# Kernel optimization log

Measured on AMD Instinct MI355X. Metric: run time of the kernel, lower is better.

Reference implementation:

```python
import math
import jax, jax.numpy as jnp
import numpy as np

B, T, E, H = 1, 2048, 2048, 16
D = E // H // 2  # head_dim = 64
DEPTH = 12
LAMBDA_INIT = 0.8 - 0.6 * math.exp(-0.3 * DEPTH)
EPS = 1e-5
NEG = -1e30


def rotary_cos_sin(seqlen, dim):
    # matches flash-attn RotaryEmbedding: inv_freq over even indices, base 10000
    inv_freq = 1.0 / (10000.0 ** (jnp.arange(0, dim, 2, dtype=jnp.float32) / dim))
    t = jnp.arange(seqlen, dtype=jnp.float32)
    freqs = jnp.outer(t, inv_freq)  # [T, D/2]
    return jnp.cos(freqs), jnp.sin(freqs)


def apply_rotary_interleaved(x, cos, sin):
    # x: [B, T, nH, D]; rotate interleaved pairs (x0,x1),(x2,x3),...
    x1 = x[..., 0::2]
    x2 = x[..., 1::2]
    c = cos[None, :, None, :]
    s = sin[None, :, None, :]
    o1 = x1 * c - x2 * s
    o2 = x1 * s + x2 * c
    return jnp.stack([o1, o2], axis=-1).reshape(x.shape)


def causal_attn_pair(q, k, v1, v2, mask, scale):
    # q,k,v*: [B, T, H, D]; shared softmax over (q,k), applied to both v1 and v2
    s = jnp.einsum('bthd,bshd->bhts', q, k) * scale
    s = jnp.where(mask, s, NEG)
    a = jax.nn.softmax(s, axis=-1)
    o1 = jnp.einsum('bhts,bshd->bthd', a, v1)
    o2 = jnp.einsum('bhts,bshd->bthd', a, v2)
    return jnp.concatenate([o1, o2], axis=-1)  # [B, T, H, 2D]


def setup_inputs() -> dict:
    key = jax.random.key(0)
    ks = jax.random.split(key, 10)
    return {
        'query': jax.random.normal(ks[0], (B, T, E), dtype=jnp.float32),
        'Wq': jax.random.normal(ks[1], (E, E), dtype=jnp.float32) * 0.02,
        'Wk': jax.random.normal(ks[2], (E, E), dtype=jnp.float32) * 0.02,
        'Wv': jax.random.normal(ks[3], (E, E), dtype=jnp.float32) * 0.02,
        'Wout': jax.random.normal(ks[4], (E, E), dtype=jnp.float32) * 0.02,
        'lambda_q1': jax.random.normal(ks[5], (D,), dtype=jnp.float32) * 0.1,
        'lambda_k1': jax.random.normal(ks[6], (D,), dtype=jnp.float32) * 0.1,
        'lambda_q2': jax.random.normal(ks[7], (D,), dtype=jnp.float32) * 0.1,
        'lambda_k2': jax.random.normal(ks[8], (D,), dtype=jnp.float32) * 0.1,
        'rms_weight': jnp.ones((2 * D,), dtype=jnp.float32),
    }


def reference(query, Wq, Wk, Wv, Wout, lambda_q1, lambda_k1, lambda_q2, lambda_k2, rms_weight):
    bsz, tgt_len, embed_dim = query.shape
    cos, sin = rotary_cos_sin(tgt_len, D)
    scale = D ** (-0.5)
    mask = jnp.tril(jnp.ones((tgt_len, tgt_len), dtype=bool))[None, None]

    q = (query @ Wq).reshape(bsz, tgt_len, 2 * H, D)
    k = (query @ Wk).reshape(bsz, tgt_len, 2 * H, D)
    v = (query @ Wv).reshape(bsz, tgt_len, H, 2, D)

    q = apply_rotary_emb = apply_rotary_interleaved(q, cos, sin)
    k = apply_rotary_interleaved(k, cos, sin)

    q = q.reshape(bsz, tgt_len, H, 2, D)
    k = k.reshape(bsz, tgt_len, H, 2, D)
    q1, q2 = q[:, :, :, 0], q[:, :, :, 1]
    k1, k2 = k[:, :, :, 0], k[:, :, :, 1]
    v1, v2 = v[:, :, :, 0], v[:, :, :, 1]

    attn1 = causal_attn_pair(q1, k1, v1, v2, mask, scale)  # [B,T,H,2D]
    attn2 = causal_attn_pair(q2, k2, v1, v2, mask, scale)

    lambda_1 = jnp.exp(jnp.sum(lambda_q1 * lambda_k1))
    lambda_2 = jnp.exp(jnp.sum(lambda_q2 * lambda_k2))
    lambda_full = lambda_1 - lambda_2 + LAMBDA_INIT

    f1 = jnp.fft.rfft(attn1, axis=1)
    f2 = jnp.fft.rfft(attn2, axis=1)
    attn_freq = f1 - lambda_full * f2

    n_freq = attn_freq.shape[1]
    sigma = 0.3 / 2.0  # cutoff_ratio / 2, gaussian window
    x = jnp.linspace(0.0, 1.0, n_freq)
    filt = jnp.exp(-0.5 * (x / sigma) ** 2)
    attn_freq = attn_freq * filt[None, :, None, None]

    attn = jnp.fft.irfft(attn_freq, n=tgt_len, axis=1)  # [B,T,H,2D]

    # RMSNorm over last dim (2*head_dim) with affine weight
    attn = attn * jax.lax.rsqrt(jnp.mean(attn * attn, axis=-1, keepdims=True) + EPS) * rms_weight
    attn = attn * (1.0 - LAMBDA_INIT)

    attn = attn.reshape(bsz, tgt_len, H * 2 * D)
    return attn @ Wout
```

## Files before the change

### kernel.cpp

```cpp
#include <hip/hip_runtime.h>
#include <math.h>

#define LAMBDA_INIT_F 0.7836057665316245f
#define ONE_MINUS_LI  0.2163942334683755f

typedef unsigned short ushort_t;
typedef unsigned int   uint32;
typedef unsigned long long u64;
typedef __attribute__((ext_vector_type(8))) short short8;
typedef __attribute__((ext_vector_type(4))) float f32x4;

__device__ __forceinline__ ushort_t f2bf(float f) {
    union { float f; uint32 u; } x; x.f = f;
    uint32 r = (x.u + 0x7fffu + ((x.u >> 16) & 1u)) >> 16;
    return (ushort_t)r;
}

__device__ __forceinline__ void gld16(ushort_t* lds, const ushort_t* g) {
    __builtin_amdgcn_global_load_lds(
        (const __attribute__((address_space(1))) uint32*)g,
        (__attribute__((address_space(3))) uint32*)lds,
        16, 0, 0);
}

__global__ __launch_bounds__(64) void lambda_kernel(
    const float* __restrict__ lq1, const float* __restrict__ lk1,
    const float* __restrict__ lq2, const float* __restrict__ lk2,
    float* __restrict__ lam)
{
    int l = threadIdx.x;
    float p1 = lq1[l] * lk1[l];
    float p2 = lq2[l] * lk2[l];
    for (int off = 32; off; off >>= 1) {
        p1 += __shfl_down(p1, off);
        p2 += __shfl_down(p2, off);
    }
    if (l == 0) lam[0] = expf(p1) - expf(p2) + LAMBDA_INIT_F;
}

__global__ __launch_bounds__(256) void gfilt_kernel(float* __restrict__ g)
{
    __shared__ float red[4];
    const int j = blockIdx.x;
    int tau = j - 64;
    int ta = tau < 0 ? -tau : tau;
    const int tid = threadIdx.x;
    float acc = 0.0f;
    for (int k = tid; k <= 1024; k += 256) {
        float w = (k == 0 || k == 1024) ? 1.0f : 2.0f;
        float r = (float)k * (1.0f / 153.6f);
        float f = expf(-0.5f * r * r);
        int m = (k * ta) & 2047;
        float ang = (float)m * 3.0679615757712823e-3f;
        acc += w * f * cosf(ang);
    }
    for (int off = 32; off; off >>= 1) acc += __shfl_down(acc, off);
    if ((tid & 63) == 0) red[tid >> 6] = acc;
    __syncthreads();
    if (tid == 0)
        g[j] = (red[0] + red[1] + red[2] + red[3]) * (1.0f / 2048.0f);
}

__global__ __launch_bounds__(256) void rottab(float* __restrict__ ct, float* __restrict__ st)
{
    int id = blockIdx.x * 256 + threadIdx.x;
    int t = id >> 5, i = id & 31;
    double inv = exp(-0.28782313662425575 * (double)i);
    double a = (double)t * inv;
    ct[id] = (float)cos(a);
    st[id] = (float)sin(a);
}

__global__ __launch_bounds__(256) void cvt_bf16(const float* __restrict__ s, ushort_t* __restrict__ d)
{
    int i = (blockIdx.x * 256 + threadIdx.x) * 8;
    float4 a = *(const float4*)(s + i);
    float4 b = *(const float4*)(s + i + 4);
    uint4 pk;
    pk.x = (uint32)f2bf(a.x) | ((uint32)f2bf(a.y) << 16);
    pk.y = (uint32)f2bf(a.z) | ((uint32)f2bf(a.w) << 16);
    pk.z = (uint32)f2bf(b.x) | ((uint32)f2bf(b.y) << 16);
    pk.w = (uint32)f2bf(b.z) | ((uint32)f2bf(b.w) << 16);
    *(uint4*)(d + i) = pk;
}

__global__ __launch_bounds__(256) void wtrans(
    const float* __restrict__ Wq, const float* __restrict__ Wk,
    const float* __restrict__ Wv, const float* __restrict__ Wo,
    ushort_t* __restrict__ Tq, ushort_t* __restrict__ Tk,
    ushort_t* __restrict__ Tv, ushort_t* __restrict__ To)
{
    int z = blockIdx.z;
    const float* S = (z == 0) ? Wq : (z == 1) ? Wk : (z == 2) ? Wv : Wo;
    ushort_t* Dt = (z == 0) ? Tq : (z == 1) ? Tk : (z == 2) ? Tv : To;
    bool perm = (z < 2);
    __shared__ float Ls[64 * 65];
    const int tid = threadIdx.x;
    const int n0 = blockIdx.x * 64, k0 = blockIdx.y * 64;
    #pragma unroll
    for (int it = 0; it < 4; ++it) {
        int kk = it * 16 + (tid >> 4);
        int nn = (tid & 15) * 4;
        float4 v = *(const float4*)(S + (size_t)(k0 + kk) * 2048 + n0 + nn);
        Ls[(nn + 0) * 65 + kk] = v.x;
        Ls[(nn + 1) * 65 + kk] = v.y;
        Ls[(nn + 2) * 65 + kk] = v.z;
        Ls[(nn + 3) * 65 + kk] = v.w;
    }
    __syncthreads();
    int nl = tid >> 2, kc = (tid & 3) * 16;
    int ng = n0 + nl;
    int nd = perm ? ((ng & ~63) | ((ng & 1) << 5) | ((ng & 63) >> 1)) : ng;
    uint4 p0, p1;
    const float* row = Ls + nl * 65 + kc;
    p0.x = (uint32)f2bf(row[0])  | ((uint32)f2bf(row[1])  << 16);
    p0.y = (uint32)f2bf(row[2])  | ((uint32)f2bf(row[3])  << 16);
    p0.z = (uint32)f2bf(row[4])  | ((uint32)f2bf(row[5])  << 16);
    p0.w = (uint32)f2bf(row[6])  | ((uint32)f2bf(row[7])  << 16);
    p1.x = (uint32)f2bf(row[8])  | ((uint32)f2bf(row[9])  << 16);
    p1.y = (uint32)f2bf(row[10]) | ((uint32)f2bf(row[11]) << 16);
    p1.z = (uint32)f2bf(row[12]) | ((uint32)f2bf(row[13]) << 16);
    p1.w = (uint32)f2bf(row[14]) | ((uint32)f2bf(row[15]) << 16);
    *(uint4*)(Dt + (size_t)nd * 2048 + k0 + kc) = p0;
    *(uint4*)(Dt + (size_t)nd * 2048 + k0 + kc + 8) = p1;
}

__global__ __launch_bounds__(256) void gemm_qkv(
    const ushort_t* __restrict__ A, const ushort_t* __restrict__ WT,
    ushort_t* __restrict__ q1, ushort_t* __restrict__ q2,
    ushort_t* __restrict__ k1, ushort_t* __restrict__ k2,
    ushort_t* __restrict__ v1T, ushort_t* __restrict__ v2T,
    const float* __restrict__ ctab, const float* __restrict__ stab)
{
    __shared__ ushort_t As[8192];
    __shared__ ushort_t Bs[8192];
    const int tid = threadIdx.x;
    const int w = tid >> 6, lane = tid & 63;
    const int quad = lane >> 4, l15 = lane & 15;
    const int wr = w >> 1, wc = w & 1;
    const int rb = blockIdx.y * 128, cb = blockIdx.x * 128;

    f32x4 acc[4][4];
    #pragma unroll
    for (int i = 0; i < 4; ++i)
        #pragma unroll
        for (int j = 0; j < 4; ++j) acc[i][j] = (f32x4)0.0f;

    for (int k0 = 0; k0 < 2048; k0 += 64) {
        #pragma unroll
        for (int u = 0; u < 4; ++u) {
            int off = (w * 4 + u) * 512;
            int Lc = (off >> 3) + lane;
            int row = Lc >> 3, cc = (Lc & 7) ^ (row & 7);
            gld16(As + off, A + (size_t)(rb + row) * 2048 + k0 + cc * 8);
            gld16(Bs + off, WT + (size_t)(cb + row) * 2048 + k0 + cc * 8);
        }
        __syncthreads();
        #pragma unroll
        for (int ks = 0; ks < 2; ++ks) {
            short8 af[4], bfr[4];
            #pragma unroll
            for (int mi = 0; mi < 4; ++mi) {
                int r = wr * 64 + mi * 16 + l15;
                af[mi] = *(const short8*)(As + r * 64 + ((ks * 4 + quad) ^ (r & 7)) * 8);
            }
            #pragma unroll
            for (int nj = 0; nj < 4; ++nj) {
                int r = wc * 64 + nj * 16 + l15;
                bfr[nj] = *(const short8*)(Bs + r * 64 + ((ks * 4 + quad) ^ (r & 7)) * 8);
            }
            #pragma unroll
            for (int mi = 0; mi < 4; ++mi)
                #pragma unroll
                for (int nj = 0; nj < 4; ++nj)
                    acc[mi][nj] = __builtin_amdgcn_mfma_f32_16x16x32_bf16(
                        af[mi], bfr[nj], acc[mi][nj], 0, 0, 0);
        }
        __syncthreads();
    }

    const int region = cb >> 11;
    const int nloc = cb & 2047;
    if (region < 2) {
        int head2 = (nloc + wc * 64) >> 6;
        ushort_t* b1 = region ? k1 : q1;
        ushort_t* b2 = region ? k2 : q2;
        ushort_t* dst = ((head2 & 1) ? b2 : b1) + (size_t)(head2 >> 1) * 2048 * 64;
        #pragma unroll
        for (int mi = 0; mi < 4; ++mi)
            #pragma unroll
            for (int r = 0; r < 4; ++r) {
                int t = rb + wr * 64 + mi * 16 + quad * 4 + r;
                const float* ctr = ctab + t * 32;
                const float* str = stab + t * 32;
                #pragma unroll
                for (int nj = 0; nj < 2; ++nj) {
                    int i = nj * 16 + l15;
                    float c = ctr[i], s = str[i];
                    float x1 = acc[mi][nj][r], x2 = acc[mi][nj + 2][r];
                    dst[(size_t)t * 64 + i]      = f2bf(x1 * c - x2 * s);
                    dst[(size_t)t * 64 + 32 + i] = f2bf(x1 * s + x2 * c);
                }
            }
    } else {
        #pragma unroll
        for (int mi = 0; mi < 4; ++mi)
            #pragma unroll
            for (int nj = 0; nj < 4; ++nj) {
                int cg = nloc + wc * 64 + nj * 16 + l15;
                int hh = cg >> 7, pr = (cg >> 6) & 1, d = cg & 63;
                int tb = rb + wr * 64 + mi * 16 + quad * 4;
                ushort_t* dst = (pr ? v2T : v1T) + ((size_t)(hh * 64 + d)) * 2048 + tb;
                u64 pk = (u64)f2bf(acc[mi][nj][0])
                       | ((u64)f2bf(acc[mi][nj][1]) << 16)
                       | ((u64)f2bf(acc[mi][nj][2]) << 32)
                       | ((u64)f2bf(acc[mi][nj][3]) << 48);
                *(u64*)dst = pk;
            }
    }
}

#define PSTRIDE 88

__device__ __forceinline__ void attn_step(
    const ushort_t* __restrict__ Kb, const ushort_t* __restrict__ V1b,
    const ushort_t* __restrict__ V2b, ushort_t* __restrict__ pw,
    const short8* qb, f32x4* O, float& m_i, float& l_i,
    int quad, int l15, int row_l, bool diag)
{
    f32x4 s[4];
    #pragma unroll
    for (int j = 0; j < 4; ++j) s[j] = (f32x4)0.0f;
    #pragma unroll
    for (int ks = 0; ks < 2; ++ks)
        #pragma unroll
        for (int j = 0; j < 4; ++j) {
            int r = j * 16 + l15;
            short8 kf = *(const short8*)(Kb + r * 64 + ((ks * 4 + quad) ^ (r & 7)) * 8);
            s[j] = __builtin_amdgcn_mfma_f32_16x16x32_bf16(kf, qb[ks], s[j], 0, 0, 0);
        }
    float pv[16];
    float mx = -1e30f;
    #pragma unroll
    for (int j = 0; j < 4; ++j)
        #pragma unroll
        for (int r = 0; r < 4; ++r) {
            float v = s[j][r] * 0.125f;
            if (diag) {
                int kp = j * 16 + quad * 4 + r;
                v = (kp <= row_l) ? v : -1e30f;
            }
            pv[j * 4 + r] = v;
            mx = fmaxf(mx, v);
        }
    mx = fmaxf(mx, __shfl_xor(mx, 16));
    mx = fmaxf(mx, __shfl_xor(mx, 32));
    float newm = fmaxf(m_i, mx);
    float alpha = __expf(m_i - newm);
    float sum = 0.0f;
    ushort_t pb[16];
    #pragma unroll
    for (int i = 0; i < 16; ++i) {
        float p = __expf(pv[i] - newm);
        sum += p;
        pb[i] = f2bf(p);
    }
    sum += __shfl_xor(sum, 16);
    sum += __shfl_xor(sum, 32);
    l_i = l_i * alpha + sum;
    m_i = newm;
    #pragma unroll
    for (int j = 0; j < 4; ++j) {
        u64 pk = (u64)pb[j * 4] | ((u64)pb[j * 4 + 1] << 16)
               | ((u64)pb[j * 4 + 2] << 32) | ((u64)pb[j * 4 + 3] << 48);
        *(u64*)(pw + l15 * PSTRIDE + j * 16 + quad * 4) = pk;
    }
    float av0 = __shfl(alpha, quad * 4 + 0);
    float av1 = __shfl(alpha, quad * 4 + 1);
    float av2 = __shfl(alpha, quad * 4 + 2);
    float av3 = __shfl(alpha, quad * 4 + 3);
    #pragma unroll
    for (int nt = 0; nt < 8; ++nt) {
        O[nt][0] *= av0; O[nt][1] *= av1; O[nt][2] *= av2; O[nt][3] *= av3;
    }
    #pragma unroll
    for (int ks = 0; ks < 2; ++ks) {
        short8 pf = *(const short8*)(pw + l15 * PSTRIDE + ks * 32 + quad * 8);
        #pragma unroll
        for (int nt = 0; nt < 8; ++nt) {
            const ushort_t* Vs = (nt < 4) ? V1b : V2b;
            int d = (nt & 3) * 16 + l15;
            short8 vf = *(const short8*)(Vs + d * 64 + ((ks * 4 + quad) ^ (d & 7)) * 8);
            O[nt] = __builtin_amdgcn_mfma_f32_16x16x32_bf16(pf, vf, O[nt], 0, 0, 0);
        }
    }
}

__global__ __launch_bounds__(256) void attn_pipe(
    const ushort_t* __restrict__ q1, const ushort_t* __restrict__ k1,
    const ushort_t* __restrict__ q2, const ushort_t* __restrict__ k2,
    const ushort_t* __restrict__ v1T, const ushort_t* __restrict__ v2T,
    float* __restrict__ X, const float* __restrict__ lam_ptr)
{
    __shared__ ushort_t Tt[4][4096];
    __shared__ ushort_t Ps[4][2][16 * PSTRIDE];

    const int tid = threadIdx.x;
    const int w = tid >> 6, lane = tid & 63;
    const int quad = lane >> 4, l15 = lane & 15;
    const int b = blockIdx.x;
    const int h = b & 15;
    const int qt = 31 - (b >> 4);
    const float lam = lam_ptr[0];
    const int row_l = w * 16 + l15;

    const ushort_t* k1h = k1 + (size_t)h * 2048 * 64;
    const ushort_t* k2h = k2 + (size_t)h * 2048 * 64;
    const ushort_t* v1h = v1T + (size_t)h * 64 * 2048;
    const ushort_t* v2h = v2T + (size_t)h * 64 * 2048;

    short8 qb1[2], qb2[2];
    {
        const ushort_t* q1p = q1 + ((size_t)h * 2048 + qt * 64 + w * 16 + l15) * 64 + quad * 8;
        const ushort_t* q2p = q2 + ((size_t)h * 2048 + qt * 64 + w * 16 + l15) * 64 + quad * 8;
        qb1[0] = *(const short8*)(q1p);      qb1[1] = *(const short8*)(q1p + 32);
        qb2[0] = *(const short8*)(q2p);      qb2[1] = *(const short8*)(q2p + 32);
    }

    int ci[2], koff[2], voff[2];
    #pragma unroll
    for (int u = 0; u < 2; ++u) {
        ci[u] = tid * 2 + u;
        int row = ci[u] >> 3, cc = (ci[u] & 7) ^ (row & 7);
        koff[u] = row * 64 + cc * 8;
        voff[u] = row * 2048 + cc * 8;
    }

    short8 sK1[2], sK2[2], sV1[2], sV2[2];

    #pragma unroll
    for (int u = 0; u < 2; ++u) {
        sK1[u] = *(const short8*)(k1h + koff[u]);
        sK2[u] = *(const short8*)(k2h + koff[u]);
        sV1[u] = *(const short8*)(v1h + voff[u]);
        sV2[u] = *(const short8*)(v2h + voff[u]);
    }
    #pragma unroll
    for (int u = 0; u < 2; ++u) {
        *(short8*)(&Tt[0][ci[u] * 8]) = sK1[u];
        *(short8*)(&Tt[1][ci[u] * 8]) = sK2[u];
        *(short8*)(&Tt[2][ci[u] * 8]) = sV1[u];
        *(short8*)(&Tt[3][ci[u] * 8]) = sV2[u];
    }
    __syncthreads();

    f32x4 O1[8], O2[8];
    #pragma unroll
    for (int i = 0; i < 8; ++i) { O1[i] = (f32x4)0.0f; O2[i] = (f32x4)0.0f; }
    float m1 = -1e30f, l1 = 0.0f, m2 = -1e30f, l2 = 0.0f;

    for (int kt = 0; kt <= qt; ++kt) {
        if (kt < qt) {
            int kb = (kt + 1) * 4096, vb = (kt + 1) * 64;
            #pragma unroll
            for (int u = 0; u < 2; ++u) {
                sK1[u] = *(const short8*)(k1h + kb + koff[u]);
                sK2[u] = *(const short8*)(k2h + kb + koff[u]);
                sV1[u] = *(const short8*)(v1h + vb + voff[u]);
                sV2[u] = *(const short8*)(v2h + vb + voff[u]);
            }
        }
        const bool diag = (kt == qt);
        attn_step(Tt[0], Tt[2], Tt[3], &Ps[w][0][0], qb1, O1, m1, l1, quad, l15, row_l, diag);
        attn_step(Tt[1], Tt[2], Tt[3], &Ps[w][1][0], qb2, O2, m2, l2, quad, l15, row_l, diag);
        __syncthreads();
        if (kt < qt) {
            #pragma unroll
            for (int u = 0; u < 2; ++u) {
                *(short8*)(&Tt[0][ci[u] * 8]) = sK1[u];
                *(short8*)(&Tt[1][ci[u] * 8]) = sK2[u];
                *(short8*)(&Tt[2][ci[u] * 8]) = sV1[u];
                *(short8*)(&Tt[3][ci[u] * 8]) = sV2[u];
            }
            __syncthreads();
        }
    }

    float r10 = 1.0f / __shfl(l1, quad * 4 + 0);
    float r11 = 1.0f / __shfl(l1, quad * 4 + 1);
    float r12 = 1.0f / __shfl(l1, quad * 4 + 2);
    float r13 = 1.0f / __shfl(l1, quad * 4 + 3);
    float r20 = lam / __shfl(l2, quad * 4 + 0);
    float r21 = lam / __shfl(l2, quad * 4 + 1);
    float r22 = lam / __shfl(l2, quad * 4 + 2);
    float r23 = lam / __shfl(l2, quad * 4 + 3);
    int tb = qt * 64 + w * 16 + quad * 4;
    #pragma unroll
    for (int nt = 0; nt < 8; ++nt) {
        int col = h * 128 + nt * 16 + l15;
        X[(size_t)(tb + 0) * 2048 + col] = O1[nt][0] * r10 - O2[nt][0] * r20;
        X[(size_t)(tb + 1) * 2048 + col] = O1[nt][1] * r11 - O2[nt][1] * r21;
        X[(size_t)(tb + 2) * 2048 + col] = O1[nt][2] * r12 - O2[nt][2] * r22;
        X[(size_t)(tb + 3) * 2048 + col] = O1[nt][3] * r13 - O2[nt][3] * r23;
    }
}

__global__ __launch_bounds__(256) void conv_t(
    const float* __restrict__ X, const float* __restrict__ g, float* __restrict__ Y)
{
    __shared__ float Xs[192 * 64];
    __shared__ float gs[129];
    const int tid = threadIdx.x;
    const int c0 = blockIdx.x * 64, t0 = blockIdx.y * 64;
    const int c = tid & 63, tg = tid >> 6;
    for (int j = tg; j < 192; j += 4)
        Xs[j * 64 + c] = X[(size_t)((t0 - 64 + j) & 2047) * 2048 + c0 + c];
    if (tid < 129) gs[tid] = g[tid];
    __syncthreads();
    float accv[16];
    #pragma unroll
    for (int i = 0; i < 16; ++i) accv[i] = 0.0f;
    const int tl0 = tg * 16;
    for (int tap = 0; tap < 129; ++tap) {
        float gv = gs[tap];
        int base = (tl0 + 128 - tap) * 64 + c;
        #pragma unroll
        for (int i = 0; i < 16; ++i) accv[i] += gv * Xs[base + i * 64];
    }
    #pragma unroll
    for (int i = 0; i < 16; ++i)
        Y[(size_t)(t0 + tl0 + i) * 2048 + c0 + c] = accv[i];
}

__global__ __launch_bounds__(64) void rms_bf(
    const float* __restrict__ Y, const float* __restrict__ wgt, ushort_t* __restrict__ yb)
{
    int grp = blockIdx.x;
    int t = grp >> 4, hh = grp & 15, l = threadIdx.x;
    size_t base = (size_t)t * 2048 + hh * 128;
    float a = Y[base + l];
    float b = Y[base + 64 + l];
    float ss = a * a + b * b;
    for (int off = 32; off; off >>= 1) ss += __shfl_down(ss, off);
    ss = __shfl(ss, 0);
    float r = rsqrtf(ss * (1.0f / 128.0f) + 1e-5f) * ONE_MINUS_LI;
    yb[base + l]      = f2bf(a * r * wgt[l]);
    yb[base + 64 + l] = f2bf(b * r * wgt[64 + l]);
}

__global__ __launch_bounds__(256) void gemm_out(
    const ushort_t* __restrict__ A, const ushort_t* __restrict__ BT,
    float* __restrict__ C)
{
    __shared__ ushort_t As[4096];
    __shared__ ushort_t Bs[8192];
    const int tid = threadIdx.x;
    const int w = tid >> 6, lane = tid & 63;
    const int quad = lane >> 4, l15 = lane & 15;
    const int wr = w >> 1, wc = w & 1;
    const int rb = blockIdx.y * 64, cb = blockIdx.x * 128;

    f32x4 acc[2][4];
    #pragma unroll
    for (int i = 0; i < 2; ++i)
        #pragma unroll
        for (int j = 0; j < 4; ++j) acc[i][j] = (f32x4)0.0f;

    for (int k0 = 0; k0 < 2048; k0 += 64) {
        #pragma unroll
        for (int u = 0; u < 2; ++u) {
            int off = (w * 2 + u) * 512;
            int Lc = (off >> 3) + lane;
            int row = Lc >> 3, cc = (Lc & 7) ^ (row & 7);
            gld16(As + off, A + (size_t)(rb + row) * 2048 + k0 + cc * 8);
        }
        #pragma unroll
        for (int u = 0; u < 4; ++u) {
            int off = (w * 4 + u) * 512;
            int Lc = (off >> 3) + lane;
            int row = Lc >> 3, cc = (Lc & 7) ^ (row & 7);
            gld16(Bs + off, BT + (size_t)(cb + row) * 2048 + k0 + cc * 8);
        }
        __syncthreads();
        #pragma unroll
        for (int ks = 0; ks < 2; ++ks) {
            short8 af[2], bfr[4];
            #pragma unroll
            for (int mi = 0; mi < 2; ++mi) {
                int r = wr * 32 + mi * 16 + l15;
                af[mi] = *(const short8*)(As + r * 64 + ((ks * 4 + quad) ^ (r & 7)) * 8);
            }
            #pragma unroll
            for (int nj = 0; nj < 4; ++nj) {
                int r = wc * 64 + nj * 16 + l15;
                bfr[nj] = *(const short8*)(Bs + r * 64 + ((ks * 4 + quad) ^ (r & 7)) * 8);
            }
            #pragma unroll
            for (int mi = 0; mi < 2; ++mi)
                #pragma unroll
                for (int nj = 0; nj < 4; ++nj)
                    acc[mi][nj] = __builtin_amdgcn_mfma_f32_16x16x32_bf16(
                        af[mi], bfr[nj], acc[mi][nj], 0, 0, 0);
        }
        __syncthreads();
    }

    #pragma unroll
    for (int mi = 0; mi < 2; ++mi)
        #pragma unroll
        for (int nj = 0; nj < 4; ++nj) {
            int cg = cb + wc * 64 + nj * 16 + l15;
            #pragma unroll
            for (int r = 0; r < 4; ++r) {
                int t = rb + wr * 32 + mi * 16 + quad * 4 + r;
                C[(size_t)t * 2048 + cg] = acc[mi][nj][r];
            }
        }
}

extern "C" void kernel_launch(void* const* d_in, const int* in_sizes, int n_in,
                              void* d_out, int out_size, void* d_ws, size_t ws_size,
                              hipStream_t stream)
{
    const float* query = (const float*)d_in[0];
    const float* Wq    = (const float*)d_in[1];
    const float* Wk    = (const float*)d_in[2];
    const float* Wv    = (const float*)d_in[3];
    const float* Wout  = (const float*)d_in[4];
    const float* lq1   = (const float*)d_in[5];
    const float* lk1   = (const float*)d_in[6];
    const float* lq2   = (const float*)d_in[7];
    const float* lk2   = (const float*)d_in[8];
    const float* rmsw  = (const float*)d_in[9];
    float* out = (float*)d_out;

    const size_t MB = 1ull << 20;
    char* W = (char*)d_ws;
    ushort_t* WqT   = (ushort_t*)(W + 0 * MB);
    ushort_t* WkT   = (ushort_t*)(W + 8 * MB);
    ushort_t* WvT   = (ushort_t*)(W + 16 * MB);
    ushort_t* WoutT = (ushort_t*)(W + 24 * MB);
    ushort_t* qb    = (ushort_t*)(W + 32 * MB);
    ushort_t* q1    = (ushort_t*)(W + 40 * MB);
    ushort_t* q2    = (ushort_t*)(W + 44 * MB);
    ushort_t* k1    = (ushort_t*)(W + 48 * MB);
    ushort_t* k2    = (ushort_t*)(W + 52 * MB);
    ushort_t* v1T   = (ushort_t*)(W + 56 * MB);
    ushort_t* v2T   = (ushort_t*)(W + 60 * MB);
    float*    X     = (float*)   (W + 64 * MB);
    float*    Y     = (float*)   (W + 32 * MB);
    ushort_t* ybf   = (ushort_t*)(W + 48 * MB);
    float*    ctab  = (float*)   (W + 80 * MB);
    float*    stab  = (float*)   (W + 80 * MB + 256 * 1024);
    float*    gbuf  = (float*)   (W + 80 * MB + 512 * 1024);
    float*    lam   = (float*)   (W + 80 * MB + 520 * 1024);

    lambda_kernel<<<1, 64, 0, stream>>>(lq1, lk1, lq2, lk2, lam);
    gfilt_kernel<<<129, 256, 0, stream>>>(gbuf);
    rottab<<<256, 256, 0, stream>>>(ctab, stab);
    cvt_bf16<<<2048, 256, 0, stream>>>(query, qb);
    wtrans<<<dim3(32, 32, 4), 256, 0, stream>>>(Wq, Wk, Wv, Wout, WqT, WkT, WvT, WoutT);

    gemm_qkv<<<dim3(48, 16), 256, 0, stream>>>(qb, WqT, q1, q2, k1, k2, v1T, v2T, ctab, stab);

    attn_pipe<<<512, 256, 0, stream>>>(q1, k1, q2, k2, v1T, v2T, X, lam);

    conv_t<<<dim3(32, 32), 256, 0, stream>>>(X, gbuf, Y);
    rms_bf<<<32768, 64, 0, stream>>>(Y, rmsw, ybf);

    gemm_out<<<dim3(16, 32), 256, 0, stream>>>(ybf, WoutT, out);
}
```

Baseline: 364.4 us.

## Split dual attention streams across separate wave groups in a 512-thread block

The attention kernel now runs 8 waves per block. Waves 0-3 compute the q1/k1 softmax path and waves 4-7 compute the q2/k2 path, where before each wave ran both paths back to back. The two results are combined through LDS at the end. The query-tile ordering also changes so that the second half of the blocks takes short tiles first, and the softmax packing is fused to avoid extra register arrays. The aim is more parallel waves and lower register pressure per wave, at the cost of an extra LDS round trip and a block barrier at the end.

```diff
diff --git a/kernel.cpp b/kernel.cpp
--- a/kernel.cpp
+++ b/kernel.cpp
@@ -239,7 +239,6 @@
             short8 kf = *(const short8*)(Kb + r * 64 + ((ks * 4 + quad) ^ (r & 7)) * 8);
             s[j] = __builtin_amdgcn_mfma_f32_16x16x32_bf16(kf, qb[ks], s[j], 0, 0, 0);
         }
-    float pv[16];
     float mx = -1e30f;
     #pragma unroll
     for (int j = 0; j < 4; ++j)
@@ -250,7 +249,7 @@
                 int kp = j * 16 + quad * 4 + r;
                 v = (kp <= row_l) ? v : -1e30f;
             }
-            pv[j * 4 + r] = v;
+            s[j][r] = v;
             mx = fmaxf(mx, v);
         }
     mx = fmaxf(mx, __shfl_xor(mx, 16));
@@ -258,23 +257,21 @@
     float newm = fmaxf(m_i, mx);
     float alpha = __expf(m_i - newm);
     float sum = 0.0f;
-    ushort_t pb[16];
-    #pragma unroll
-    for (int i = 0; i < 16; ++i) {
-        float p = __expf(pv[i] - newm);
-        sum += p;
-        pb[i] = f2bf(p);
+    #pragma unroll
+    for (int j = 0; j < 4; ++j) {
+        float p0 = __expf(s[j][0] - newm);
+        float p1 = __expf(s[j][1] - newm);
+        float p2 = __expf(s[j][2] - newm);
+        float p3 = __expf(s[j][3] - newm);
+        sum += (p0 + p1) + (p2 + p3);
+        u64 pk = (u64)f2bf(p0) | ((u64)f2bf(p1) << 16)
+               | ((u64)f2bf(p2) << 32) | ((u64)f2bf(p3) << 48);
+        *(u64*)(pw + l15 * PSTRIDE + j * 16 + quad * 4) = pk;
     }
     sum += __shfl_xor(sum, 16);
     sum += __shfl_xor(sum, 32);
     l_i = l_i * alpha + sum;
     m_i = newm;
-    #pragma unroll
-    for (int j = 0; j < 4; ++j) {
-        u64 pk = (u64)pb[j * 4] | ((u64)pb[j * 4 + 1] << 16)
-               | ((u64)pb[j * 4 + 2] << 32) | ((u64)pb[j * 4 + 3] << 48);
-        *(u64*)(pw + l15 * PSTRIDE + j * 16 + quad * 4) = pk;
-    }
     float av0 = __shfl(alpha, quad * 4 + 0);
     float av1 = __shfl(alpha, quad * 4 + 1);
     float av2 = __shfl(alpha, quad * 4 + 2);
@@ -296,112 +293,113 @@
     }
 }
 
-__global__ __launch_bounds__(256) void attn_pipe(
+__global__ __launch_bounds__(512, 4) void attn_pipe(
     const ushort_t* __restrict__ q1, const ushort_t* __restrict__ k1,
     const ushort_t* __restrict__ q2, const ushort_t* __restrict__ k2,
     const ushort_t* __restrict__ v1T, const ushort_t* __restrict__ v2T,
     float* __restrict__ X, const float* __restrict__ lam_ptr)
 {
     __shared__ ushort_t Tt[4][4096];
-    __shared__ ushort_t Ps[4][2][16 * PSTRIDE];
+    __shared__ ushort_t Ps[8][16 * PSTRIDE];
 
     const int tid = threadIdx.x;
     const int w = tid >> 6, lane = tid & 63;
     const int quad = lane >> 4, l15 = lane & 15;
+    const int pair = w >> 2, wl = w & 3;
     const int b = blockIdx.x;
     const int h = b & 15;
-    const int qt = 31 - (b >> 4);
+    const int x16 = (b & 255) >> 4;
+    const int qt = (b < 256) ? (31 - x16) : x16;
     const float lam = lam_ptr[0];
-    const int row_l = w * 16 + l15;
+    const int row_l = wl * 16 + l15;
 
     const ushort_t* k1h = k1 + (size_t)h * 2048 * 64;
     const ushort_t* k2h = k2 + (size_t)h * 2048 * 64;
     const ushort_t* v1h = v1T + (size_t)h * 64 * 2048;
     const ushort_t* v2h = v2T + (size_t)h * 64 * 2048;
 
-    short8 qb1[2], qb2[2];
+    short8 qb[2];
     {
-        const ushort_t* q1p = q1 + ((size_t)h * 2048 + qt * 64 + w * 16 + l15) * 64 + quad * 8;
-        const ushort_t* q2p = q2 + ((size_t)h * 2048 + qt * 64 + w * 16 + l15) * 64 + quad * 8;
-        qb1[0] = *(const short8*)(q1p);      qb1[1] = *(const short8*)(q1p + 32);
-        qb2[0] = *(const short8*)(q2p);      qb2[1] = *(const short8*)(q2p + 32);
-    }
-
-    int ci[2], koff[2], voff[2];
-    #pragma unroll
-    for (int u = 0; u < 2; ++u) {
-        ci[u] = tid * 2 + u;
-        int row = ci[u] >> 3, cc = (ci[u] & 7) ^ (row & 7);
-        koff[u] = row * 64 + cc * 8;
-        voff[u] = row * 2048 + cc * 8;
-    }
-
-    short8 sK1[2], sK2[2], sV1[2], sV2[2];
-
-    #pragma unroll
-    for (int u = 0; u < 2; ++u) {
-        sK1[u] = *(const short8*)(k1h + koff[u]);
-        sK2[u] = *(const short8*)(k2h + koff[u]);
-        sV1[u] = *(const short8*)(v1h + voff[u]);
-        sV2[u] = *(const short8*)(v2h + voff[u]);
-    }
-    #pragma unroll
-    for (int u = 0; u < 2; ++u) {
-        *(short8*)(&Tt[0][ci[u] * 8]) = sK1[u];
-        *(short8*)(&Tt[1][ci[u] * 8]) = sK2[u];
-        *(short8*)(&Tt[2][ci[u] * 8]) = sV1[u];
-        *(short8*)(&Tt[3][ci[u] * 8]) = sV2[u];
-    }
+        const ushort_t* qp = (pair ? q2 : q1)
+            + ((size_t)h * 2048 + qt * 64 + wl * 16 + l15) * 64 + quad * 8;
+        qb[0] = *(const short8*)(qp);
+        qb[1] = *(const short8*)(qp + 32);
+    }
+
+    const int ci = tid;
+    const int srow = ci >> 3, scc = (ci & 7) ^ (srow & 7);
+    const int koff = srow * 64 + scc * 8;
+    const int voff = srow * 2048 + scc * 8;
+
+    short8 sK1, sK2, sV1, sV2;
+
+    sK1 = *(const short8*)(k1h + koff);
+    sK2 = *(const short8*)(k2h + koff);
+    sV1 = *(const short8*)(v1h + voff);
+    sV2 = *(const short8*)(v2h + voff);
+    *(short8*)(&Tt[0][ci * 8]) = sK1;
+    *(short8*)(&Tt[1][ci * 8]) = sK2;
+    *(short8*)(&Tt[2][ci * 8]) = sV1;
+    *(short8*)(&Tt[3][ci * 8]) = sV2;
     __syncthreads();
 
-    f32x4 O1[8], O2[8];
-    #pragma unroll
-    for (int i = 0; i < 8; ++i) { O1[i] = (f32x4)0.0f; O2[i] = (f32x4)0.0f; }
-    float m1 = -1e30f, l1 = 0.0f, m2 = -1e30f, l2 = 0.0f;
+    f32x4 O[8];
+    #pragma unroll
+    for (int i = 0; i < 8; ++i) O[i] = (f32x4)0.0f;
+    float m_i = -1e30f, l_i = 0.0f;
+
+    const ushort_t* Kb = Tt[pair];
 
     for (int kt = 0; kt <= qt; ++kt) {
         if (kt < qt) {
             int kb = (kt + 1) * 4096, vb = (kt + 1) * 64;
-            #pragma unroll
-            for (int u = 0; u < 2; ++u) {
-                sK1[u] = *(const short8*)(k1h + kb + koff[u]);
-                sK2[u] = *(const short8*)(k2h + kb + koff[u]);
-                sV1[u] = *(const short8*)(v1h + vb + voff[u]);
-                sV2[u] = *(const short8*)(v2h + vb + voff[u]);
-            }
-        }
-        const bool diag = (kt == qt);
-        attn_step(Tt[0], Tt[2], Tt[3], &Ps[w][0][0], qb1, O1, m1, l1, quad, l15, row_l, diag);
-        attn_step(Tt[1], Tt[2], Tt[3], &Ps[w][1][0], qb2, O2, m2, l2, quad, l15, row_l, diag);
+            sK1 = *(const short8*)(k1h + kb + koff);
+            sK2 = *(const short8*)(k2h + kb + koff);
+            sV1 = *(const short8*)(v1h + vb + voff);
+            sV2 = *(const short8*)(v2h + vb + voff);
+        }
+        attn_step(Kb, Tt[2], Tt[3], &Ps[w][0], qb, O, m_i, l_i,
+                  quad, l15, row_l, kt == qt);
         __syncthreads();
         if (kt < qt) {
-            #pragma unroll
-            for (int u = 0; u < 2; ++u) {
-                *(short8*)(&Tt[0][ci[u] * 8]) = sK1[u];
-                *(short8*)(&Tt[1][ci[u] * 8]) = sK2[u];
-                *(short8*)(&Tt[2][ci[u] * 8]) = sV1[u];
-                *(short8*)(&Tt[3][ci[u] * 8]) = sV2[u];
-            }
+            *(short8*)(&Tt[0][ci * 8]) = sK1;
+            *(short8*)(&Tt[1][ci * 8]) = sK2;
+            *(short8*)(&Tt[2][ci * 8]) = sV1;
+            *(short8*)(&Tt[3][ci * 8]) = sV2;
             __syncthreads();
         }
     }
 
-    float r10 = 1.0f / __shfl(l1, quad * 4 + 0);
-    float r11 = 1.0f / __shfl(l1, quad * 4 + 1);
-    float r12 = 1.0f / __shfl(l1, quad * 4 + 2);
-    float r13 = 1.0f / __shfl(l1, quad * 4 + 3);
-    float r20 = lam / __shfl(l2, quad * 4 + 0);
-    float r21 = lam / __shfl(l2, quad * 4 + 1);
-    float r22 = lam / __shfl(l2, quad * 4 + 2);
-    float r23 = lam / __shfl(l2, quad * 4 + 3);
-    int tb = qt * 64 + w * 16 + quad * 4;
-    #pragma unroll
-    for (int nt = 0; nt < 8; ++nt) {
-        int col = h * 128 + nt * 16 + l15;
-        X[(size_t)(tb + 0) * 2048 + col] = O1[nt][0] * r10 - O2[nt][0] * r20;
-        X[(size_t)(tb + 1) * 2048 + col] = O1[nt][1] * r11 - O2[nt][1] * r21;
-        X[(size_t)(tb + 2) * 2048 + col] = O1[nt][2] * r12 - O2[nt][2] * r22;
-        X[(size_t)(tb + 3) * 2048 + col] = O1[nt][3] * r13 - O2[nt][3] * r23;
+    float sc = pair ? lam : 1.0f;
+    float rr0 = sc / __shfl(l_i, quad * 4 + 0);
+    float rr1 = sc / __shfl(l_i, quad * 4 + 1);
+    float rr2 = sc / __shfl(l_i, quad * 4 + 2);
+    float rr3 = sc / __shfl(l_i, quad * 4 + 3);
+
+    float* LX = (float*)&Tt[0][0];
+    const int rbase = wl * 16 + quad * 4;
+    if (pair) {
+        #pragma unroll
+        for (int nt = 0; nt < 8; ++nt) {
+            int cb = nt * 16 + l15;
+            LX[(rbase + 0) * 128 + cb] = O[nt][0] * rr0;
+            LX[(rbase + 1) * 128 + cb] = O[nt][1] * rr1;
+            LX[(rbase + 2) * 128 + cb] = O[nt][2] * rr2;
+            LX[(rbase + 3) * 128 + cb] = O[nt][3] * rr3;
+        }
+    }
+    __syncthreads();
+    if (!pair) {
+        int tb = qt * 64 + rbase;
+        #pragma unroll
+        for (int nt = 0; nt < 8; ++nt) {
+            int cb = nt * 16 + l15;
+            int col = h * 128 + cb;
+            X[(size_t)(tb + 0) * 2048 + col] = O[nt][0] * rr0 - LX[(rbase + 0) * 128 + cb];
+            X[(size_t)(tb + 1) * 2048 + col] = O[nt][1] * rr1 - LX[(rbase + 1) * 128 + cb];
+            X[(size_t)(tb + 2) * 2048 + col] = O[nt][2] * rr2 - LX[(rbase + 2) * 128 + cb];
+            X[(size_t)(tb + 3) * 2048 + col] = O[nt][3] * rr3 - LX[(rbase + 3) * 128 + cb];
+        }
     }
 }
 
@@ -563,7 +561,7 @@
 
     gemm_qkv<<<dim3(48, 16), 256, 0, stream>>>(qb, WqT, q1, q2, k1, k2, v1T, v2T, ctab, stab);
 
-    attn_pipe<<<512, 256, 0, stream>>>(q1, k1, q2, k2, v1T, v2T, X, lam);
+    attn_pipe<<<512, 512, 0, stream>>>(q1, k1, q2, k2, v1T, v2T, X, lam);
 
     conv_t<<<dim3(32, 32), 256, 0, stream>>>(X, gbuf, Y);
     rms_bf<<<32768, 64, 0, stream>>>(Y, rmsw, ybf);
```

Result: faster. 344.0 us (-5.6%).
